# Performance work log

Hardware: AMD Instinct MI355X
Metric: run time of the kernel (lower is better)

The kernel has to match this reference:

```python
import jax, jax.numpy as jnp
import numpy as np

D_MODEL = 1024
D_FF = 4096
N_EXPERTS = 8
TOP_K = 2

def setup_inputs() -> dict:
    key = jax.random.key(0)
    ks = jax.random.split(key, 8)
    s = 0.02
    return {
        "x": jax.random.normal(ks[0], (4, 2048, D_MODEL), dtype=jnp.float32),
        "W1": jax.random.normal(ks[1], (N_EXPERTS, D_MODEL, D_FF), dtype=jnp.float32) * s,
        "b1": jnp.zeros((N_EXPERTS, D_FF), dtype=jnp.float32),
        "W2": jax.random.normal(ks[2], (N_EXPERTS, D_FF, D_MODEL), dtype=jnp.float32) * s,
        "b2": jnp.zeros((N_EXPERTS, D_MODEL), dtype=jnp.float32),
        "Wg": jax.random.normal(ks[3], (D_MODEL, N_EXPERTS), dtype=jnp.float32) * s,
        "bg": jnp.zeros((N_EXPERTS,), dtype=jnp.float32),
    }

def reference(x, W1, b1, W2, b2, Wg, bg):
    B, S, D = x.shape
    # Gating network
    gate_logits = jnp.einsum('bsd,de->bse', x, Wg) + bg
    gate_probs = jax.nn.softmax(gate_logits, axis=-1)  # (B,S,E)
    # Top-k routing on softmax probs (matches torch.topk(F.softmax(logits)))
    top_k_probs, top_k_indices = jax.lax.top_k(gate_probs, TOP_K)  # (B,S,k)
    T = B * S
    x_flat = x.reshape(T, D)
    idx_flat = top_k_indices.reshape(T, TOP_K)
    prob_flat = top_k_probs.reshape(T, TOP_K)
    # Per-token combine weight for each expert: sum of top-k probs routed to it
    # combine[t, e] = sum_j prob_flat[t, j] * (idx_flat[t, j] == e)
    onehot = jax.nn.one_hot(idx_flat, N_EXPERTS, dtype=x.dtype)  # (T,k,E)
    combine = jnp.einsum('tk,tke->te', prob_flat, onehot)  # (T,E)
    out = jnp.zeros((T, D), dtype=x.dtype)
    for e in range(N_EXPERTS):  # static small loop over experts
        h = jax.nn.relu(x_flat @ W1[e] + b1[e])  # (T, d_ff)
        y = h @ W2[e] + b2[e]                    # (T, d_model)
        out = out + combine[:, e:e+1] * y
    return out.reshape(B, S, D), gate_probs
```

## Files before the change

kernel.cpp:

```cpp
#include <hip/hip_runtime.h>

#define D_MODEL 1024
#define D_FF    4096
#define N_EXP   8
#define BM 256
#define BN 256
#define BK 64

typedef __attribute__((ext_vector_type(8))) short bf16x8;
typedef __attribute__((ext_vector_type(4))) float f32x4;
typedef unsigned int u32;

__device__ __forceinline__ unsigned short f2bf(float f) {
  union { float f; unsigned u; } v; v.f = f;
  unsigned r = v.u + 0x7FFFu + ((v.u >> 16) & 1u);
  return (unsigned short)(r >> 16);
}

__device__ __forceinline__ void gl_lds16(const void* g, void* l) {
  __builtin_amdgcn_global_load_lds((const __attribute__((address_space(1))) u32*)g,
                                   (__attribute__((address_space(3))) u32*)l, 16, 0, 0);
}

__global__ void convert_x_kernel(const float* __restrict__ x,
                                 unsigned short* __restrict__ xb, int total8) {
  int i = blockIdx.x * blockDim.x + threadIdx.x;
  if (i >= total8) return;
  const float4* src = (const float4*)x + (size_t)i * 2;
  float4 a = src[0], b = src[1];
  ushort4 lo, hi;
  lo.x = f2bf(a.x); lo.y = f2bf(a.y); lo.z = f2bf(a.z); lo.w = f2bf(a.w);
  hi.x = f2bf(b.x); hi.y = f2bf(b.y); hi.z = f2bf(b.z); hi.w = f2bf(b.w);
  ushort4* dst = (ushort4*)xb + (size_t)i * 2;
  dst[0] = lo; dst[1] = hi;
}

__global__ __launch_bounds__(256)
void transpose_convert_kernel(const float* __restrict__ src, unsigned short* __restrict__ dst,
                              int Ksub, int Nsrc, int k0, int n0, int Nchunk,
                              unsigned long long eStride) {
  __shared__ unsigned short s[64][65];
  int e = blockIdx.z;
  int kb = blockIdx.x * 64, nb = blockIdx.y * 64;
  const float* se = src + (size_t)e * eStride;
  unsigned short* de = dst + (size_t)e * Nchunk * Ksub;
  int tid = threadIdx.x;
  int lk = tid >> 4, ln = (tid & 15) * 4;
  #pragma unroll
  for (int p = 0; p < 4; p++) {
    int k = lk + p * 16;
    float4 v = *(const float4*)(se + (size_t)(k0 + kb + k) * Nsrc + (n0 + nb + ln));
    s[ln + 0][k] = f2bf(v.x);
    s[ln + 1][k] = f2bf(v.y);
    s[ln + 2][k] = f2bf(v.z);
    s[ln + 3][k] = f2bf(v.w);
  }
  __syncthreads();
  #pragma unroll
  for (int c = 0; c < 2; c++) {
    int id = tid + c * 256;
    int n = id >> 3, kc = id & 7;
    unsigned short u[8];
    #pragma unroll
    for (int j = 0; j < 8; j++) u[j] = s[n][kc * 8 + j];
    *(uint4*)(de + (size_t)(nb + n) * Ksub + kb + kc * 8) = *(const uint4*)u;
  }
}

__global__ void gating_kernel(const float* __restrict__ x,
                              const float* __restrict__ Wg,
                              const float* __restrict__ bg,
                              float* __restrict__ gate_out,
                              int* __restrict__ cnt,
                              int* __restrict__ tokIdx,
                              float* __restrict__ tokW, int T) {
  int wv = threadIdx.x >> 6, lane = threadIdx.x & 63;
  int t = blockIdx.x * 4 + wv;
  if (t >= T) return;
  const float* xr = x + (size_t)t * D_MODEL + lane * 16;
  float acc[N_EXP];
  #pragma unroll
  for (int e = 0; e < N_EXP; e++) acc[e] = 0.f;
  #pragma unroll
  for (int q = 0; q < 4; q++) {
    float4 xv = *(const float4*)(xr + q * 4);
    #pragma unroll
    for (int r = 0; r < 4; r++) {
      float xs = ((const float*)&xv)[r];
      const float* wrow = Wg + (size_t)(lane * 16 + q * 4 + r) * N_EXP;
      float4 wa = *(const float4*)wrow;
      float4 wb = *(const float4*)(wrow + 4);
      acc[0] += xs * wa.x; acc[1] += xs * wa.y; acc[2] += xs * wa.z; acc[3] += xs * wa.w;
      acc[4] += xs * wb.x; acc[5] += xs * wb.y; acc[6] += xs * wb.z; acc[7] += xs * wb.w;
    }
  }
  #pragma unroll
  for (int off = 32; off > 0; off >>= 1) {
    #pragma unroll
    for (int e = 0; e < N_EXP; e++) acc[e] += __shfl_xor(acc[e], off);
  }
  if (lane == 0) {
    float l[N_EXP], p[N_EXP];
    float m = -1e30f;
    #pragma unroll
    for (int e = 0; e < N_EXP; e++) { l[e] = acc[e] + bg[e]; m = fmaxf(m, l[e]); }
    float s = 0.f;
    #pragma unroll
    for (int e = 0; e < N_EXP; e++) { p[e] = __expf(l[e] - m); s += p[e]; }
    float inv = 1.f / s;
    #pragma unroll
    for (int e = 0; e < N_EXP; e++) { p[e] *= inv; gate_out[(size_t)t * N_EXP + e] = p[e]; }
    int e1 = 0;
    #pragma unroll
    for (int e = 1; e < N_EXP; e++) if (p[e] > p[e1]) e1 = e;
    int e2 = (e1 == 0) ? 1 : 0;
    #pragma unroll
    for (int e = 0; e < N_EXP; e++) if (e != e1 && p[e] > p[e2]) e2 = e;
    int pos = atomicAdd(cnt + e1, 1);
    tokIdx[(size_t)e1 * T + pos] = t; tokW[(size_t)e1 * T + pos] = p[e1];
    pos = atomicAdd(cnt + e2, 1);
    tokIdx[(size_t)e2 * T + pos] = t; tokW[(size_t)e2 * T + pos] = p[e2];
  }
}

__global__ void schedule_kernel(const int* __restrict__ cnt, int* __restrict__ meta,
                                int* __restrict__ tE, int* __restrict__ tB,
                                int* __restrict__ tV, int T, int maxTiles) {
  if (threadIdx.x != 0 || blockIdx.x != 0) return;
  int t = 0;
  for (int e = 0; e < N_EXP; e++) {
    int c = cnt[e];
    for (int r = 0; r < c && t < maxTiles; r += BM) {
      tE[t] = e; tB[t] = e * T + r; tV[t] = min(BM, c - r); t++;
    }
  }
  meta[0] = t;
}

#define STAGE(bufbase, kt) do { \
    _Pragma("unroll") for (int c_ = 0; c_ < 4; c_++) { \
      gl_lds16(srcA[c_] + (size_t)(kt) * BK, (bufbase) + (w * 32 + c_ * 8) * 64); \
      gl_lds16(srcB[c_] + (size_t)(kt) * BK, (bufbase) + 16384 + (w * 32 + c_ * 8) * 64); } \
  } while (0)

#define RD_A(cur, qm) { _Pragma("unroll") for (int m_ = 0; m_ < 4; m_++) { \
    int row_ = (qm) * 128 + wm64 + m_ * 16 + l15; \
    _Pragma("unroll") for (int kk_ = 0; kk_ < 2; kk_++) \
      a[m_][kk_] = *(const bf16x8*)&(cur)[row_ * 64 + (((kk_ * 4 + l4 + row_) & 7) << 3)]; } }

#define RD_B(cur, qn, bb) { _Pragma("unroll") for (int n_ = 0; n_ < 2; n_++) { \
    int rb_ = (qn) * 128 + wn32 + n_ * 16 + l15; \
    _Pragma("unroll") for (int kk_ = 0; kk_ < 2; kk_++) \
      bb[n_][kk_] = *(const bf16x8*)&(cur)[16384 + rb_ * 64 + (((kk_ * 4 + l4 + rb_) & 7) << 3)]; } }

#define MQ(qm, qn, bb) { _Pragma("unroll") for (int m_ = 0; m_ < 4; m_++) \
    _Pragma("unroll") for (int n_ = 0; n_ < 2; n_++) { \
      acc[qm][qn][m_][n_] = __builtin_amdgcn_mfma_f32_16x16x32_bf16(a[m_][0], bb[n_][0], acc[qm][qn][m_][n_], 0, 0, 0); \
      acc[qm][qn][m_][n_] = __builtin_amdgcn_mfma_f32_16x16x32_bf16(a[m_][1], bb[n_][1], acc[qm][qn][m_][n_], 0, 0, 0); } }

#define KLOOP(NT) \
  STAGE(As, 0); \
  asm volatile("s_waitcnt vmcnt(0)" ::: "memory"); \
  __builtin_amdgcn_sched_barrier(0); \
  __builtin_amdgcn_s_barrier(); \
  __builtin_amdgcn_sched_barrier(0); \
  for (int kt = 0; kt < (NT); kt++) { \
    unsigned short* cur = As + (kt & 1) * 32768; \
    unsigned short* nxt = As + ((kt + 1) & 1) * 32768; \
    if (kt + 1 < (NT)) STAGE(nxt, kt + 1); \
    __builtin_amdgcn_sched_barrier(0); \
    RD_A(cur, 0); RD_B(cur, 0, b0); RD_B(cur, 1, b1); \
    MQ(0, 0, b0); MQ(0, 1, b1); \
    RD_A(cur, 1); \
    MQ(1, 1, b1); MQ(1, 0, b0); \
    __builtin_amdgcn_sched_barrier(0); \
    asm volatile("s_waitcnt vmcnt(0)" ::: "memory"); \
    __builtin_amdgcn_sched_barrier(0); \
    __builtin_amdgcn_s_barrier(); \
    __builtin_amdgcn_sched_barrier(0); \
  }

#define ACC_INIT() f32x4 acc[2][2][4][2]; \
  _Pragma("unroll") for (int qm = 0; qm < 2; qm++) \
    _Pragma("unroll") for (int qn = 0; qn < 2; qn++) \
      _Pragma("unroll") for (int m = 0; m < 4; m++) \
        _Pragma("unroll") for (int n = 0; n < 2; n++) acc[qm][qn][m][n] = (f32x4){0.f, 0.f, 0.f, 0.f};

__global__ __launch_bounds__(512, 2)
void gemm1_kernel(const unsigned short* __restrict__ xb,
                  const unsigned short* __restrict__ w1t,
                  const float* __restrict__ b1,
                  const int* __restrict__ meta,
                  const int* __restrict__ tE, const int* __restrict__ tB,
                  const int* __restrict__ tV, const int* __restrict__ tokIdx,
                  unsigned short* __restrict__ hbuf, int FFC, int chunk_off, int ncolLog2) {
  __shared__ unsigned short As[65536];

  int total = gridDim.x;
  int L = blockIdx.x;
  int q = total >> 3, r8 = total & 7;
  int xcd = L & 7, idx = L >> 3;
  int work = (xcd < r8) ? (xcd * (q + 1) + idx) : (r8 * (q + 1) + (xcd - r8) * q + idx);
  int ncol = 1 << ncolLog2;
  int tile = work >> ncolLog2;
  int cb = work & (ncol - 1);
  if (tile >= meta[0]) return;
  int e = tE[tile], base = tB[tile], valid = tV[tile];
  int tid = threadIdx.x;

  int w = tid >> 6, lane = tid & 63;
  int wm = w >> 2, wn = w & 3;
  int wm64 = wm * 64, wn32 = wn * 32;
  int l15 = lane & 15, l4 = lane >> 4;
  int sr = lane >> 3, scg = lane & 7;

  const unsigned short* panel = w1t + (size_t)e * FFC * D_MODEL;
  const unsigned short* srcA[4];
  const unsigned short* srcB[4];
  #pragma unroll
  for (int c = 0; c < 4; c++) {
    int r = w * 32 + c * 8 + sr;
    int rc = r < valid ? r : valid - 1;
    int tok = tokIdx[base + rc];
    int swz = ((scg - r) & 7) << 3;
    srcA[c] = xb + (size_t)tok * D_MODEL + swz;
    srcB[c] = panel + (size_t)(cb * BN + r) * D_MODEL + swz;
  }

  ACC_INIT();
  bf16x8 a[4][2], b0[2][2], b1f[2][2];
  #define b1 b1f
  KLOOP(D_MODEL / BK);
  #undef b1

  const float* b1e = b1 + (size_t)e * D_FF + chunk_off + cb * BN;
  #pragma unroll
  for (int qn = 0; qn < 2; qn++)
    #pragma unroll
    for (int n = 0; n < 2; n++) {
      int colL = qn * 128 + wn32 + n * 16 + l15;
      float bias = b1e[colL];
      #pragma unroll
      for (int qm = 0; qm < 2; qm++)
        #pragma unroll
        for (int m = 0; m < 4; m++)
          #pragma unroll
          for (int r = 0; r < 4; r++) {
            int row = qm * 128 + wm64 + m * 16 + l4 * 4 + r;
            float v = acc[qm][qn][m][n][r] + bias;
            v = v > 0.f ? v : 0.f;
            hbuf[(size_t)(tile * BM + row) * FFC + cb * BN + colL] = f2bf(v);
          }
    }
}

__global__ __launch_bounds__(512, 2)
void gemm2_kernel(const unsigned short* __restrict__ hbuf,
                  const unsigned short* __restrict__ w2t,
                  const float* __restrict__ b2,
                  const int* __restrict__ meta,
                  const int* __restrict__ tE, const int* __restrict__ tB,
                  const int* __restrict__ tV, const int* __restrict__ tokIdx,
                  const float* __restrict__ tokW,
                  float* __restrict__ out, int FFC, int chunk) {
  __shared__ unsigned short As[65536];

  int total = gridDim.x;
  int L = blockIdx.x;
  int q = total >> 3, r8 = total & 7;
  int xcd = L & 7, idx = L >> 3;
  int work = (xcd < r8) ? (xcd * (q + 1) + idx) : (r8 * (q + 1) + (xcd - r8) * q + idx);
  int tile = work >> 3;
  int cb = (work >> 1) & 3;
  int ks = work & 1;
  if (tile >= meta[0]) return;
  int e = tE[tile], base = tB[tile], valid = tV[tile];
  int tid = threadIdx.x;

  int w = tid >> 6, lane = tid & 63;
  int wm = w >> 2, wn = w & 3;
  int wm64 = wm * 64, wn32 = wn * 32;
  int l15 = lane & 15, l4 = lane >> 4;
  int sr = lane >> 3, scg = lane & 7;

  const int nt = FFC / BK / 2;
  const int ksOff = ks * nt * BK;

  const unsigned short* panel = w2t + (size_t)e * D_MODEL * FFC;
  const unsigned short* srcA[4];
  const unsigned short* srcB[4];
  #pragma unroll
  for (int c = 0; c < 4; c++) {
    int r = w * 32 + c * 8 + sr;
    int swz = ((scg - r) & 7) << 3;
    srcA[c] = hbuf + (size_t)(tile * BM + r) * FFC + ksOff + swz;
    srcB[c] = panel + (size_t)(cb * BN + r) * FFC + ksOff + swz;
  }

  ACC_INIT();
  bf16x8 a[4][2], b0[2][2], b1[2][2];
  KLOOP(nt);

  int addBias = (chunk == 0 && ks == 0) ? 1 : 0;
  #pragma unroll
  for (int qn = 0; qn < 2; qn++)
    #pragma unroll
    for (int n = 0; n < 2; n++) {
      int colg = cb * BN + qn * 128 + wn32 + n * 16 + l15;
      float bias = addBias ? b2[(size_t)e * D_MODEL + colg] : 0.f;
      #pragma unroll
      for (int qm = 0; qm < 2; qm++)
        #pragma unroll
        for (int m = 0; m < 4; m++)
          #pragma unroll
          for (int r = 0; r < 4; r++) {
            int row = qm * 128 + wm64 + m * 16 + l4 * 4 + r;
            if (row < valid) {
              float wgt = tokW[base + row];
              int tok = tokIdx[base + row];
              float v = (acc[qm][qn][m][n][r] + bias) * wgt;
              atomicAdd(out + (size_t)tok * D_MODEL + colg, v);
            }
          }
    }
}

extern "C" void kernel_launch(void* const* d_in, const int* in_sizes, int n_in,
                              void* d_out, int out_size, void* d_ws, size_t ws_size,
                              hipStream_t stream) {
  const float* x  = (const float*)d_in[0];
  const float* W1 = (const float*)d_in[1];
  const float* b1 = (const float*)d_in[2];
  const float* W2 = (const float*)d_in[3];
  const float* b2 = (const float*)d_in[4];
  const float* Wg = (const float*)d_in[5];
  const float* bg = (const float*)d_in[6];

  int T = in_sizes[0] / D_MODEL;
  float* out = (float*)d_out;
  float* gate_out = out + (size_t)T * D_MODEL;

  char* ws = (char*)d_ws;
  int* cnt  = (int*)(ws + 0);
  int* meta = (int*)(ws + 64);
  int* tE   = (int*)(ws + 128);
  int* tB   = (int*)(ws + 1024);
  int* tV   = (int*)(ws + 2048);
  size_t off = 4096;
  int* tokIdx = (int*)(ws + off);   off += (size_t)N_EXP * T * 4;
  float* tokW = (float*)(ws + off); off += (size_t)N_EXP * T * 4;
  unsigned short* xb = (unsigned short*)(ws + off); off += (size_t)T * D_MODEL * 2;
  off = (off + 255) & ~(size_t)255;

  int maxTiles = (2 * T) / BM + N_EXP;
  int FFC = D_FF;
  while (FFC > 256 &&
         off + (size_t)FFC * (16384 + 16384 + (size_t)maxTiles * BM * 2) > ws_size)
    FFC >>= 1;

  unsigned short* w1t = (unsigned short*)(ws + off); off += (size_t)FFC * 16384;
  unsigned short* w2t = (unsigned short*)(ws + off); off += (size_t)FFC * 16384;
  unsigned short* h   = (unsigned short*)(ws + off);

  hipMemsetAsync(d_out, 0, (size_t)T * D_MODEL * sizeof(float), stream);
  hipMemsetAsync(cnt, 0, N_EXP * sizeof(int), stream);

  int total8 = T * D_MODEL / 8;
  convert_x_kernel<<<(total8 + 255) / 256, 256, 0, stream>>>(x, xb, total8);
  gating_kernel<<<(T + 3) / 4, 256, 0, stream>>>(x, Wg, bg, gate_out, cnt, tokIdx, tokW, T);
  schedule_kernel<<<1, 64, 0, stream>>>(cnt, meta, tE, tB, tV, T, maxTiles);

  int ncol1 = FFC / BN;
  int ncol1Log2 = __builtin_ctz(ncol1);
  for (int c = 0; c * FFC < D_FF; c++) {
    transpose_convert_kernel<<<dim3(D_MODEL / 64, FFC / 64, N_EXP), 256, 0, stream>>>(
        W1, w1t, D_MODEL, D_FF, 0, c * FFC, FFC, (unsigned long long)D_MODEL * D_FF);
    transpose_convert_kernel<<<dim3(FFC / 64, D_MODEL / 64, N_EXP), 256, 0, stream>>>(
        W2, w2t, FFC, D_MODEL, c * FFC, 0, D_MODEL, (unsigned long long)D_FF * D_MODEL);
    gemm1_kernel<<<maxTiles * ncol1, 512, 0, stream>>>(
        xb, w1t, b1, meta, tE, tB, tV, tokIdx, h, FFC, c * FFC, ncol1Log2);
    gemm2_kernel<<<maxTiles * (D_MODEL / BN) * 2, 512, 0, stream>>>(
        h, w2t, b2, meta, tE, tB, tV, tokIdx, tokW, out, FFC, c);
  }
}
```

Before: 836.2 us.

## Halve K tile to cut LDS footprint, split GEMM2 K four ways, cache token metadata

Reduces BK from 64 to 32, halving the double-buffered LDS footprint from 128KB to 64KB, with a new 4-way swizzle for the narrower rows. It also drops the sched_barrier fences in favour of s_setprio around the MFMA section and an unroll-2 k loop. GEMM2 now splits the FF reduction four ways instead of two, doubling its grid, and stages token indices and weights in LDS for the atomic epilogue. Risks include more barriers per unit of work, shorter k-steps, and twice the atomic traffic into the output.

Result: slower. 1.035 ms (+23.8%).

```diff
diff --git a/kernel.cpp b/kernel.cpp
--- a/kernel.cpp
+++ b/kernel.cpp
@@ -5,7 +5,7 @@
 #define N_EXP   8
 #define BM 256
 #define BN 256
-#define BK 64
+#define BK 32
 
 typedef __attribute__((ext_vector_type(8))) short bf16x8;
 typedef __attribute__((ext_vector_type(4))) float f32x4;
@@ -137,47 +137,38 @@
   meta[0] = t;
 }
 
-#define STAGE(bufbase, kt) do { \
-    _Pragma("unroll") for (int c_ = 0; c_ < 4; c_++) { \
-      gl_lds16(srcA[c_] + (size_t)(kt) * BK, (bufbase) + (w * 32 + c_ * 8) * 64); \
-      gl_lds16(srcB[c_] + (size_t)(kt) * BK, (bufbase) + 16384 + (w * 32 + c_ * 8) * 64); } \
-  } while (0)
-
-#define RD_A(cur, qm) { _Pragma("unroll") for (int m_ = 0; m_ < 4; m_++) { \
+#define STAGE(bsel, kt) { _Pragma("unroll") for (int p_ = 0; p_ < 2; p_++) { \
+    gl_lds16(srcA[p_] + (size_t)(kt) * BK, &LDSU[(bsel) * 16384 + (w * 32 + p_ * 16) * 32]); \
+    gl_lds16(srcB[p_] + (size_t)(kt) * BK, &LDSU[(bsel) * 16384 + 8192 + (w * 32 + p_ * 16) * 32]); } }
+
+#define RD_A(bsel, qm) { _Pragma("unroll") for (int m_ = 0; m_ < 4; m_++) { \
     int row_ = (qm) * 128 + wm64 + m_ * 16 + l15; \
-    _Pragma("unroll") for (int kk_ = 0; kk_ < 2; kk_++) \
-      a[m_][kk_] = *(const bf16x8*)&(cur)[row_ * 64 + (((kk_ * 4 + l4 + row_) & 7) << 3)]; } }
-
-#define RD_B(cur, qn, bb) { _Pragma("unroll") for (int n_ = 0; n_ < 2; n_++) { \
+    a[m_] = *(const bf16x8*)&LDSU[(bsel) * 16384 + row_ * 32 + (((l4 + row_ + (row_ >> 2)) & 3) << 3)]; } }
+
+#define RD_B(bsel, qn, bb) { _Pragma("unroll") for (int n_ = 0; n_ < 2; n_++) { \
     int rb_ = (qn) * 128 + wn32 + n_ * 16 + l15; \
-    _Pragma("unroll") for (int kk_ = 0; kk_ < 2; kk_++) \
-      bb[n_][kk_] = *(const bf16x8*)&(cur)[16384 + rb_ * 64 + (((kk_ * 4 + l4 + rb_) & 7) << 3)]; } }
+    bb[n_] = *(const bf16x8*)&LDSU[(bsel) * 16384 + 8192 + rb_ * 32 + (((l4 + rb_ + (rb_ >> 2)) & 3) << 3)]; } }
 
 #define MQ(qm, qn, bb) { _Pragma("unroll") for (int m_ = 0; m_ < 4; m_++) \
-    _Pragma("unroll") for (int n_ = 0; n_ < 2; n_++) { \
-      acc[qm][qn][m_][n_] = __builtin_amdgcn_mfma_f32_16x16x32_bf16(a[m_][0], bb[n_][0], acc[qm][qn][m_][n_], 0, 0, 0); \
-      acc[qm][qn][m_][n_] = __builtin_amdgcn_mfma_f32_16x16x32_bf16(a[m_][1], bb[n_][1], acc[qm][qn][m_][n_], 0, 0, 0); } }
+    _Pragma("unroll") for (int n_ = 0; n_ < 2; n_++) \
+      acc[qm][qn][m_][n_] = __builtin_amdgcn_mfma_f32_16x16x32_bf16(a[m_], bb[n_], acc[qm][qn][m_][n_], 0, 0, 0); }
 
 #define KLOOP(NT) \
-  STAGE(As, 0); \
+  STAGE(0, 0); \
   asm volatile("s_waitcnt vmcnt(0)" ::: "memory"); \
-  __builtin_amdgcn_sched_barrier(0); \
   __builtin_amdgcn_s_barrier(); \
-  __builtin_amdgcn_sched_barrier(0); \
+  _Pragma("unroll 2") \
   for (int kt = 0; kt < (NT); kt++) { \
-    unsigned short* cur = As + (kt & 1) * 32768; \
-    unsigned short* nxt = As + ((kt + 1) & 1) * 32768; \
-    if (kt + 1 < (NT)) STAGE(nxt, kt + 1); \
-    __builtin_amdgcn_sched_barrier(0); \
-    RD_A(cur, 0); RD_B(cur, 0, b0); RD_B(cur, 1, b1); \
-    MQ(0, 0, b0); MQ(0, 1, b1); \
-    RD_A(cur, 1); \
-    MQ(1, 1, b1); MQ(1, 0, b0); \
-    __builtin_amdgcn_sched_barrier(0); \
+    int bsel = kt & 1; \
+    if (kt + 1 < (NT)) STAGE(1 - bsel, kt + 1); \
+    __builtin_amdgcn_s_setprio(1); \
+    RD_A(bsel, 0); RD_B(bsel, 0, fb0); RD_B(bsel, 1, fb1); \
+    MQ(0, 0, fb0); MQ(0, 1, fb1); \
+    RD_A(bsel, 1); \
+    MQ(1, 1, fb1); MQ(1, 0, fb0); \
+    __builtin_amdgcn_s_setprio(0); \
     asm volatile("s_waitcnt vmcnt(0)" ::: "memory"); \
-    __builtin_amdgcn_sched_barrier(0); \
     __builtin_amdgcn_s_barrier(); \
-    __builtin_amdgcn_sched_barrier(0); \
   }
 
 #define ACC_INIT() f32x4 acc[2][2][4][2]; \
@@ -189,12 +180,12 @@
 __global__ __launch_bounds__(512, 2)
 void gemm1_kernel(const unsigned short* __restrict__ xb,
                   const unsigned short* __restrict__ w1t,
-                  const float* __restrict__ b1,
+                  const float* __restrict__ bias1,
                   const int* __restrict__ meta,
                   const int* __restrict__ tE, const int* __restrict__ tB,
                   const int* __restrict__ tV, const int* __restrict__ tokIdx,
                   unsigned short* __restrict__ hbuf, int FFC, int chunk_off, int ncolLog2) {
-  __shared__ unsigned short As[65536];
+  __shared__ unsigned short LDSU[32768];
 
   int total = gridDim.x;
   int L = blockIdx.x;
@@ -212,28 +203,26 @@
   int wm = w >> 2, wn = w & 3;
   int wm64 = wm * 64, wn32 = wn * 32;
   int l15 = lane & 15, l4 = lane >> 4;
-  int sr = lane >> 3, scg = lane & 7;
+  int sr4 = lane >> 2, c_lds = lane & 3;
 
   const unsigned short* panel = w1t + (size_t)e * FFC * D_MODEL;
-  const unsigned short* srcA[4];
-  const unsigned short* srcB[4];
-  #pragma unroll
-  for (int c = 0; c < 4; c++) {
-    int r = w * 32 + c * 8 + sr;
+  const unsigned short* srcA[2];
+  const unsigned short* srcB[2];
+  #pragma unroll
+  for (int p = 0; p < 2; p++) {
+    int r = w * 32 + p * 16 + sr4;
     int rc = r < valid ? r : valid - 1;
     int tok = tokIdx[base + rc];
-    int swz = ((scg - r) & 7) << 3;
-    srcA[c] = xb + (size_t)tok * D_MODEL + swz;
-    srcB[c] = panel + (size_t)(cb * BN + r) * D_MODEL + swz;
+    int g = (c_lds - r - (r >> 2)) & 3;
+    srcA[p] = xb + (size_t)tok * D_MODEL + g * 8;
+    srcB[p] = panel + (size_t)(cb * BN + r) * D_MODEL + g * 8;
   }
 
   ACC_INIT();
-  bf16x8 a[4][2], b0[2][2], b1f[2][2];
-  #define b1 b1f
+  bf16x8 a[4], fb0[2], fb1[2];
   KLOOP(D_MODEL / BK);
-  #undef b1
-
-  const float* b1e = b1 + (size_t)e * D_FF + chunk_off + cb * BN;
+
+  const float* b1e = bias1 + (size_t)e * D_FF + chunk_off + cb * BN;
   #pragma unroll
   for (int qn = 0; qn < 2; qn++)
     #pragma unroll
@@ -257,48 +246,56 @@
 __global__ __launch_bounds__(512, 2)
 void gemm2_kernel(const unsigned short* __restrict__ hbuf,
                   const unsigned short* __restrict__ w2t,
-                  const float* __restrict__ b2,
+                  const float* __restrict__ bias2,
                   const int* __restrict__ meta,
                   const int* __restrict__ tE, const int* __restrict__ tB,
                   const int* __restrict__ tV, const int* __restrict__ tokIdx,
                   const float* __restrict__ tokW,
                   float* __restrict__ out, int FFC, int chunk) {
-  __shared__ unsigned short As[65536];
+  __shared__ unsigned short LDSU[32768];
+  __shared__ int stok[BM];
+  __shared__ float swt[BM];
 
   int total = gridDim.x;
   int L = blockIdx.x;
   int q = total >> 3, r8 = total & 7;
   int xcd = L & 7, idx = L >> 3;
   int work = (xcd < r8) ? (xcd * (q + 1) + idx) : (r8 * (q + 1) + (xcd - r8) * q + idx);
-  int tile = work >> 3;
-  int cb = (work >> 1) & 3;
-  int ks = work & 1;
+  int tile = work >> 4;
+  int cb = (work >> 2) & 3;
+  int ks = work & 3;
   if (tile >= meta[0]) return;
   int e = tE[tile], base = tB[tile], valid = tV[tile];
   int tid = threadIdx.x;
+
+  if (tid < BM) {
+    int rr = tid < valid ? tid : valid - 1;
+    stok[tid] = tokIdx[base + rr];
+    swt[tid] = tokW[base + rr];
+  }
 
   int w = tid >> 6, lane = tid & 63;
   int wm = w >> 2, wn = w & 3;
   int wm64 = wm * 64, wn32 = wn * 32;
   int l15 = lane & 15, l4 = lane >> 4;
-  int sr = lane >> 3, scg = lane & 7;
-
-  const int nt = FFC / BK / 2;
+  int sr4 = lane >> 2, c_lds = lane & 3;
+
+  const int nt = FFC / BK / 4;
   const int ksOff = ks * nt * BK;
 
   const unsigned short* panel = w2t + (size_t)e * D_MODEL * FFC;
-  const unsigned short* srcA[4];
-  const unsigned short* srcB[4];
-  #pragma unroll
-  for (int c = 0; c < 4; c++) {
-    int r = w * 32 + c * 8 + sr;
-    int swz = ((scg - r) & 7) << 3;
-    srcA[c] = hbuf + (size_t)(tile * BM + r) * FFC + ksOff + swz;
-    srcB[c] = panel + (size_t)(cb * BN + r) * FFC + ksOff + swz;
+  const unsigned short* srcA[2];
+  const unsigned short* srcB[2];
+  #pragma unroll
+  for (int p = 0; p < 2; p++) {
+    int r = w * 32 + p * 16 + sr4;
+    int g = (c_lds - r - (r >> 2)) & 3;
+    srcA[p] = hbuf + (size_t)(tile * BM + r) * FFC + ksOff + g * 8;
+    srcB[p] = panel + (size_t)(cb * BN + r) * FFC + ksOff + g * 8;
   }
 
   ACC_INIT();
-  bf16x8 a[4][2], b0[2][2], b1[2][2];
+  bf16x8 a[4], fb0[2], fb1[2];
   KLOOP(nt);
 
   int addBias = (chunk == 0 && ks == 0) ? 1 : 0;
@@ -307,7 +304,7 @@
     #pragma unroll
     for (int n = 0; n < 2; n++) {
       int colg = cb * BN + qn * 128 + wn32 + n * 16 + l15;
-      float bias = addBias ? b2[(size_t)e * D_MODEL + colg] : 0.f;
+      float bias = addBias ? bias2[(size_t)e * D_MODEL + colg] : 0.f;
       #pragma unroll
       for (int qm = 0; qm < 2; qm++)
         #pragma unroll
@@ -316,10 +313,8 @@
           for (int r = 0; r < 4; r++) {
             int row = qm * 128 + wm64 + m * 16 + l4 * 4 + r;
             if (row < valid) {
-              float wgt = tokW[base + row];
-              int tok = tokIdx[base + row];
-              float v = (acc[qm][qn][m][n][r] + bias) * wgt;
-              atomicAdd(out + (size_t)tok * D_MODEL + colg, v);
+              float v = (acc[qm][qn][m][n][r] + bias) * swt[row];
+              atomicAdd(out + (size_t)stok[row] * D_MODEL + colg, v);
             }
           }
     }
@@ -379,7 +374,7 @@
         W2, w2t, FFC, D_MODEL, c * FFC, 0, D_MODEL, (unsigned long long)D_FF * D_MODEL);
     gemm1_kernel<<<maxTiles * ncol1, 512, 0, stream>>>(
         xb, w1t, b1, meta, tE, tB, tV, tokIdx, h, FFC, c * FFC, ncol1Log2);
-    gemm2_kernel<<<maxTiles * (D_MODEL / BN) * 2, 512, 0, stream>>>(
+    gemm2_kernel<<<maxTiles * 4 * 4, 512, 0, stream>>>(
         h, w2t, b2, meta, tE, tB, tV, tokIdx, tokW, out, FFC, c);
   }
 }
```
